# Kernel optimization log

Measured on AMD Instinct MI355X. Metric: run time of the kernel, lower is better.

Reference implementation:

```python
import jax, jax.numpy as jnp
import numpy as np

D = 3
NUM_LEVELS = 16
LEVEL_DIM = 2
BASE_RES = 16
PER_LEVEL_SCALE = 2.0
LOG2_HASH = 19
MAX_PARAMS = 2 ** LOG2_HASH
BASIS_NUM = 8
N_POINTS = 524288
N_FRAMES = 4

# per-level resolution / table-size bookkeeping, exactly as in ExpHashEncoder.__init__
_res = [int(np.ceil(BASE_RES * PER_LEVEL_SCALE ** l)) for l in range(NUM_LEVELS)]
_params = [int(min(MAX_PARAMS, (r + 1) ** D)) for r in _res]
_offsets = np.concatenate([[0], np.cumsum(_params)]).astype(np.int64)
TOTAL_PARAMS = int(_offsets[-1])  # 7131219

_PRIMES = np.array([1, 2654435761, 805459861], dtype=np.uint32)  # torch-ngp fast_hash primes
_CORNERS = np.stack(np.meshgrid(np.arange(2), np.arange(2), np.arange(2), indexing='ij'), -1).reshape(-1, D).astype(np.int32)  # [8,3]


def setup_inputs() -> dict:
    key = jax.random.key(0)
    k1, k2, k3, k4, k5 = jax.random.split(key, 5)
    inputs = jax.random.uniform(k1, (N_POINTS, D), dtype=jnp.float32)  # points in [0,1)^3
    exp = jax.random.normal(k2, (N_FRAMES, BASIS_NUM), dtype=jnp.float32)
    xyzstorays = jax.random.randint(k3, (N_POINTS,), 0, N_FRAMES * 1024, dtype=jnp.int32)
    std = 1e-4  # matches reset_parameters uniform(-1e-4, 1e-4)
    embeddings_mean = (jax.random.uniform(k4, (1, TOTAL_PARAMS, LEVEL_DIM), dtype=jnp.float32) * 2 - 1) * std
    embeddings = (jax.random.uniform(k5, (BASIS_NUM - 1, TOTAL_PARAMS, LEVEL_DIM), dtype=jnp.float32) * 2 - 1) * std
    return {"inputs": inputs, "exp": exp, "embeddings_mean": embeddings_mean,
            "embeddings": embeddings, "xyzstorays": xyzstorays}


def _grid_encode(inputs, cur_emb, frames):
    # inputs [B,3] in [0,1]; cur_emb [F, TOTAL_PARAMS, C]; frames [B] int32
    corners = jnp.asarray(_CORNERS)          # [8,3]
    primes = jnp.asarray(_PRIMES)            # [3] uint32
    outs = []
    for l in range(NUM_LEVELS):
        res, hsize, off = _res[l], _params[l], int(_offsets[l])
        scale = BASE_RES * PER_LEVEL_SCALE ** l - 1.0  # kernel: exp2(l*S)*H - 1
        pos = inputs * scale + 0.5            # [B,3]
        pg = jnp.floor(pos)
        frac = pos - pg                       # [B,3] trilinear fractions
        cc = pg.astype(jnp.int32)[:, None, :] + corners[None]  # [B,8,3] corner coords
        # trilinear weights: prod_d (bit_d ? frac_d : 1-frac_d)
        w = jnp.prod(jnp.where(corners[None].astype(bool), frac[:, None, :], 1.0 - frac[:, None, :]), axis=-1)  # [B,8]
        if (res + 1) ** D <= hsize:
            # dense (tiled) indexing with stride (res+1), as in get_grid_index
            stride = res + 1
            idx = cc[..., 0] + cc[..., 1] * stride + cc[..., 2] * (stride * stride)
        else:
            # fast_hash: xor of coord*prime, uint32 wraparound, then mod table size
            cu = cc.astype(jnp.uint32)
            h = (cu[..., 0] * primes[0]) ^ (cu[..., 1] * primes[1]) ^ (cu[..., 2] * primes[2])
            idx = (h % jnp.uint32(hsize)).astype(jnp.int32)
        emb_l = jax.lax.dynamic_slice_in_dim(cur_emb, off, hsize, axis=1)  # [F,hsize,C]
        vals = emb_l[frames[:, None], idx]    # [B,8,C] per-frame gather
        outs.append(jnp.sum(w[..., None] * vals, axis=1))  # [B,C]
    return jnp.concatenate(outs, axis=-1)     # [B, L*C]


def reference(inputs, exp, embeddings_mean, embeddings, xyzstorays):
    frames = (xyzstorays // 1024).astype(jnp.int32)  # [B]
    basis = jnp.concatenate([embeddings_mean, embeddings], axis=0)  # [BASIS, T, C]
    cur = jnp.einsum('fb,btc->ftc', exp, basis)                     # blended per-frame tables [F,T,C]
    return _grid_encode(inputs, cur, frames)
```

## Files before the change

### kernel.cpp

```cpp
#include <hip/hip_runtime.h>
#include <hip/hip_bf16.h>
#include <stdint.h>


static constexpr int      NPOINTS = 524288;
static constexpr size_t   TOTAL_T = 7131219;
static constexpr uint32_t NENT    = 7131219u;
static constexpr uint32_t TPAD    = 7131264;
static constexpr uint32_t BLEND_BLOCKS = (NENT + 1023u) / 1024u;

#define OFFS_INIT {0u,4913u,40850u,315475u,839763u,1364051u,1888339u,2412627u, \
                   2936915u,3461203u,3985491u,4509779u,5034067u,5558355u,6082643u,6606931u}

__device__ __forceinline__ uint32_t pack_bf16x2(float a, float b) {
    __hip_bfloat162 h;
    h.x = __float2bfloat16(a);
    h.y = __float2bfloat16(b);
    uint32_t u;
    __builtin_memcpy(&u, &h, 4);
    return u;
}

__device__ __forceinline__ float2 unpack_bf16x2(uint32_t u) {
    float2 r;
    uint32_t lx = u << 16;
    uint32_t ly = u & 0xFFFF0000u;
    __builtin_memcpy(&r.x, &lx, 4);
    __builtin_memcpy(&r.y, &ly, 4);
    return r;
}

__device__ __forceinline__ float2 nt_load_f2(const float2* p) {
    uint64_t raw = __builtin_nontemporal_load((const uint64_t*)p);
    float2 r;
    __builtin_memcpy(&r, &raw, 8);
    return r;
}

__global__ __launch_bounds__(256) void blend_coal_kernel(
    const float2* __restrict__ mean2, const float2* __restrict__ emb2,
    const float* __restrict__ expw, uint32_t* __restrict__ cur)
{
    float w[4][8];
#pragma unroll
    for (int f = 0; f < 4; ++f)
#pragma unroll
        for (int b = 0; b < 8; ++b)
            w[f][b] = expw[8 * f + b];

    uint32_t base = blockIdx.x * 1024u + threadIdx.x;

    if (blockIdx.x != BLEND_BLOCKS - 1u) {
#pragma unroll
        for (int k = 0; k < 4; ++k) {
            uint32_t idx = base + 256u * k;
            float2 m = nt_load_f2(&mean2[idx]);
            float ax[4], ay[4];
#pragma unroll
            for (int f = 0; f < 4; ++f) { ax[f] = w[f][0] * m.x; ay[f] = w[f][0] * m.y; }
#pragma unroll
            for (int b = 0; b < 7; ++b) {
                float2 v = nt_load_f2(&emb2[(size_t)b * TOTAL_T + idx]);
#pragma unroll
                for (int f = 0; f < 4; ++f) {
                    ax[f] = fmaf(w[f][b + 1], v.x, ax[f]);
                    ay[f] = fmaf(w[f][b + 1], v.y, ay[f]);
                }
            }
#pragma unroll
            for (int f = 0; f < 4; ++f)
                cur[(size_t)f * TPAD + idx] = pack_bf16x2(ax[f], ay[f]);
        }
    } else {
#pragma unroll
        for (int k = 0; k < 4; ++k) {
            uint32_t idx = base + 256u * k;
            if (idx >= NENT) return;
            float2 m = nt_load_f2(&mean2[idx]);
            float ax[4], ay[4];
#pragma unroll
            for (int f = 0; f < 4; ++f) { ax[f] = w[f][0] * m.x; ay[f] = w[f][0] * m.y; }
#pragma unroll
            for (int b = 0; b < 7; ++b) {
                float2 v = nt_load_f2(&emb2[(size_t)b * TOTAL_T + idx]);
#pragma unroll
                for (int f = 0; f < 4; ++f) {
                    ax[f] = fmaf(w[f][b + 1], v.x, ax[f]);
                    ay[f] = fmaf(w[f][b + 1], v.y, ay[f]);
                }
            }
#pragma unroll
            for (int f = 0; f < 4; ++f)
                cur[(size_t)f * TPAD + idx] = pack_bf16x2(ax[f], ay[f]);
        }
    }
}

__global__ __launch_bounds__(256) void gather_lvl_kernel(
    const float* __restrict__ xyz, const int* __restrict__ rays,
    const uint32_t* __restrict__ cur, float* __restrict__ out)
{
    uint32_t phase = blockIdx.x >> 11;
    uint32_t pb    = blockIdx.x & 2047u;
    uint32_t p     = pb * 256u + threadIdx.x;

    float x = xyz[3 * p + 0], y = xyz[3 * p + 1], z = xyz[3 * p + 2];
    uint32_t frame = ((uint32_t)rays[p]) >> 10;
    const uint32_t* __restrict__ tab = cur + (size_t)frame * TPAD;

    if (phase == 0) {
        float o[6];
        const uint32_t ST[3]  = {17u, 33u, 65u};
        const uint32_t OFF[3] = {0u, 4913u, 40850u};
#pragma unroll
        for (int l = 0; l < 3; ++l) {
            float scale = (float)((16 << l) - 1);
            float px = fmaf(x, scale, 0.5f);
            float py = fmaf(y, scale, 0.5f);
            float pz = fmaf(z, scale, 0.5f);
            float fx = floorf(px), fy = floorf(py), fz = floorf(pz);
            float wx = px - fx, wy = py - fy, wz = pz - fz;
            uint32_t ix = (uint32_t)(int)fx, iy = (uint32_t)(int)fy, iz = (uint32_t)(int)fz;
            uint32_t st = ST[l], st2 = st * st, base = OFF[l];
            float sx = 0.f, sy = 0.f;
#pragma unroll
            for (int c = 0; c < 8; ++c) {
                uint32_t bx = (c >> 2) & 1, by = (c >> 1) & 1, bz = c & 1;
                uint32_t idx = base + (ix + bx) + (iy + by) * st + (iz + bz) * st2;
                float w = (bx ? wx : 1.f - wx) * (by ? wy : 1.f - wy) * (bz ? wz : 1.f - wz);
                float2 v = unpack_bf16x2(tab[idx]);
                sx = fmaf(w, v.x, sx);
                sy = fmaf(w, v.y, sy);
            }
            o[2 * l] = sx; o[2 * l + 1] = sy;
        }
        float* ob = out + (size_t)p * 32;
        *(float4*)ob       = make_float4(o[0], o[1], o[2], o[3]);
        *(float2*)(ob + 4) = make_float2(o[4], o[5]);
    } else {
        int l = (int)phase + 2;
        float scale = (float)((16 << l) - 1);
        uint32_t base = 315475u + ((phase - 1u) << 19);
        float px = fmaf(x, scale, 0.5f);
        float py = fmaf(y, scale, 0.5f);
        float pz = fmaf(z, scale, 0.5f);
        float fx = floorf(px), fy = floorf(py), fz = floorf(pz);
        float wx = px - fx, wy = py - fy, wz = pz - fz;
        uint32_t ix = (uint32_t)(int)fx, iy = (uint32_t)(int)fy, iz = (uint32_t)(int)fz;
        float sx = 0.f, sy = 0.f;
#pragma unroll
        for (int c = 0; c < 8; ++c) {
            uint32_t bx = (c >> 2) & 1, by = (c >> 1) & 1, bz = c & 1;
            uint32_t h = (ix + bx)
                       ^ ((iy + by) * 2654435761u)
                       ^ ((iz + bz) * 805459861u);
            uint32_t idx = base + (h & 0x7FFFFu);
            float w = (bx ? wx : 1.f - wx) * (by ? wy : 1.f - wy) * (bz ? wz : 1.f - wz);
            float2 v = unpack_bf16x2(tab[idx]);
            sx = fmaf(w, v.x, sx);
            sy = fmaf(w, v.y, sy);
        }
        *(float2*)(out + (size_t)p * 32 + 2 * l) = make_float2(sx, sy);
    }
}

__global__ __launch_bounds__(256) void fused_fallback_kernel(
    const float* __restrict__ xyz, const int* __restrict__ rays,
    const float* __restrict__ expw,
    const float2* __restrict__ mean, const float2* __restrict__ emb,
    float* __restrict__ out)
{
    int p = blockIdx.x * 256 + threadIdx.x;
    if (p >= NPOINTS) return;
    float x = xyz[3 * p], y = xyz[3 * p + 1], z = xyz[3 * p + 2];
    int frame = rays[p] >> 10;
    float e[8];
#pragma unroll
    for (int b = 0; b < 8; ++b) e[b] = expw[8 * frame + b];

    constexpr uint32_t OFFS[16] = OFFS_INIT;

    for (int l = 0; l < 16; ++l) {
        float scale = (float)((16 << l) - 1);
        float px = fmaf(x, scale, 0.5f);
        float py = fmaf(y, scale, 0.5f);
        float pz = fmaf(z, scale, 0.5f);
        float fx = floorf(px), fy = floorf(py), fz = floorf(pz);
        float wx = px - fx, wy = py - fy, wz = pz - fz;
        int ix = (int)fx, iy = (int)fy, iz = (int)fz;
        uint32_t base = OFFS[l];
        float sx = 0.f, sy = 0.f;
#pragma unroll
        for (int c = 0; c < 8; ++c) {
            int bx = (c >> 2) & 1, by = (c >> 1) & 1, bz = c & 1;
            uint32_t idx;
            if (l < 3) {
                uint32_t st = (l == 0) ? 17u : (l == 1) ? 33u : 65u;
                idx = (uint32_t)(ix + bx) + (uint32_t)(iy + by) * st
                    + (uint32_t)(iz + bz) * st * st;
            } else {
                idx = ((uint32_t)(ix + bx)
                     ^ ((uint32_t)(iy + by) * 2654435761u)
                     ^ ((uint32_t)(iz + bz) * 805459861u)) & 0x7FFFFu;
            }
            uint32_t g = base + idx;
            float2 m = mean[g];
            float vx = e[0] * m.x, vy = e[0] * m.y;
#pragma unroll
            for (int b = 0; b < 7; ++b) {
                float2 t = emb[(size_t)b * TOTAL_T + g];
                vx = fmaf(e[1 + b], t.x, vx);
                vy = fmaf(e[1 + b], t.y, vy);
            }
            float w = (bx ? wx : 1.f - wx) * (by ? wy : 1.f - wy) * (bz ? wz : 1.f - wz);
            sx = fmaf(w, vx, sx);
            sy = fmaf(w, vy, sy);
        }
        out[(size_t)p * 32 + 2 * l]     = sx;
        out[(size_t)p * 32 + 2 * l + 1] = sy;
    }
}

extern "C" void kernel_launch(void* const* d_in, const int* in_sizes, int n_in,
                              void* d_out, int out_size, void* d_ws, size_t ws_size,
                              hipStream_t stream) {
    const float* inputs = (const float*)d_in[0];
    const float* expw   = (const float*)d_in[1];
    const float* mean   = (const float*)d_in[2];
    const float* emb    = (const float*)d_in[3];
    const int*   rays   = (const int*)d_in[4];
    float* out = (float*)d_out;

    const size_t need_bf16 = (size_t)4 * TPAD * 4;

    if (ws_size >= need_bf16) {
        uint32_t* cur = (uint32_t*)d_ws;
        blend_coal_kernel<<<BLEND_BLOCKS, 256, 0, stream>>>(
            (const float2*)mean, (const float2*)emb, expw, cur);
        gather_lvl_kernel<<<14 * 2048, 256, 0, stream>>>(
            inputs, rays, cur, out);
    } else {
        fused_fallback_kernel<<<NPOINTS / 256, 256, 0, stream>>>(
            inputs, rays, expw, (const float2*)mean, (const float2*)emb, out);
    }
}
```

Baseline: 1.051 ms.

## Sort points by frame before gathering and add batched-load blend with merge pass

Adds a counting sort that groups points by frame into a packed xyz+index buffer. The per-level gather then reads one frame table per block group and writes level-major results to workspace, and a merge kernel scatters those rows back into the output. The blend kernel now issues all 32 loads per thread before doing any FMAs, to raise memory-level parallelism. This is meant to improve cache locality of the random table lookups. In exchange it adds extra kernels, workspace traffic and an output permutation, and it only runs if the workspace is large enough.

```diff
diff --git a/kernel.cpp b/kernel.cpp
--- a/kernel.cpp
+++ b/kernel.cpp
@@ -8,6 +8,14 @@
 static constexpr uint32_t NENT    = 7131219u;
 static constexpr uint32_t TPAD    = 7131264;
 static constexpr uint32_t BLEND_BLOCKS = (NENT + 1023u) / 1024u;
+
+static constexpr size_t OFF_CUR   = 0;
+static constexpr size_t OFF_SXYZF = 114100224;
+static constexpr size_t OFF_SPERM = OFF_SXYZF + 8388608;
+static constexpr size_t OFF_CTRS  = OFF_SPERM + 2097152;
+static constexpr size_t OFF_WS    = OFF_CTRS + 256;
+static constexpr size_t NEED_V4   = OFF_WS + 67108864;
+static constexpr size_t NEED_V3   = 114100224;
 
 #define OFFS_INIT {0u,4913u,40850u,315475u,839763u,1364051u,1888339u,2412627u, \
                    2936915u,3461203u,3985491u,4509779u,5034067u,5558355u,6082643u,6606931u}
@@ -37,7 +45,7 @@
     return r;
 }
 
-__global__ __launch_bounds__(256) void blend_coal_kernel(
+__global__ __launch_bounds__(256) void blend_mlp_kernel(
     const float2* __restrict__ mean2, const float2* __restrict__ emb2,
     const float* __restrict__ expw, uint32_t* __restrict__ cur)
 {
@@ -51,52 +59,194 @@
     uint32_t base = blockIdx.x * 1024u + threadIdx.x;
 
     if (blockIdx.x != BLEND_BLOCKS - 1u) {
+        float2 v[4][8];
 #pragma unroll
         for (int k = 0; k < 4; ++k) {
             uint32_t idx = base + 256u * k;
-            float2 m = nt_load_f2(&mean2[idx]);
+            v[k][0] = nt_load_f2(&mean2[idx]);
+#pragma unroll
+            for (int b = 0; b < 7; ++b)
+                v[k][1 + b] = nt_load_f2(&emb2[(size_t)b * TOTAL_T + idx]);
+        }
+#pragma unroll
+        for (int k = 0; k < 4; ++k) {
+            uint32_t idx = base + 256u * k;
             float ax[4], ay[4];
 #pragma unroll
+            for (int f = 0; f < 4; ++f) { ax[f] = w[f][0] * v[k][0].x; ay[f] = w[f][0] * v[k][0].y; }
+#pragma unroll
+            for (int b = 0; b < 7; ++b)
+#pragma unroll
+                for (int f = 0; f < 4; ++f) {
+                    ax[f] = fmaf(w[f][b + 1], v[k][1 + b].x, ax[f]);
+                    ay[f] = fmaf(w[f][b + 1], v[k][1 + b].y, ay[f]);
+                }
+#pragma unroll
+            for (int f = 0; f < 4; ++f)
+                cur[(size_t)f * TPAD + idx] = pack_bf16x2(ax[f], ay[f]);
+        }
+    } else {
+#pragma unroll
+        for (int k = 0; k < 4; ++k) {
+            uint32_t idx = base + 256u * k;
+            if (idx >= NENT) continue;
+            float2 m = mean2[idx];
+            float ax[4], ay[4];
+#pragma unroll
             for (int f = 0; f < 4; ++f) { ax[f] = w[f][0] * m.x; ay[f] = w[f][0] * m.y; }
 #pragma unroll
             for (int b = 0; b < 7; ++b) {
-                float2 v = nt_load_f2(&emb2[(size_t)b * TOTAL_T + idx]);
+                float2 e = emb2[(size_t)b * TOTAL_T + idx];
 #pragma unroll
                 for (int f = 0; f < 4; ++f) {
-                    ax[f] = fmaf(w[f][b + 1], v.x, ax[f]);
-                    ay[f] = fmaf(w[f][b + 1], v.y, ay[f]);
+                    ax[f] = fmaf(w[f][b + 1], e.x, ax[f]);
+                    ay[f] = fmaf(w[f][b + 1], e.y, ay[f]);
                 }
             }
 #pragma unroll
             for (int f = 0; f < 4; ++f)
                 cur[(size_t)f * TPAD + idx] = pack_bf16x2(ax[f], ay[f]);
         }
+    }
+}
+
+__global__ void sort_init_kernel(uint32_t* ctrs) {
+    if (threadIdx.x < 16) ctrs[threadIdx.x] = 0u;
+}
+
+__global__ __launch_bounds__(256) void sort_count_kernel(
+    const int* __restrict__ rays, uint32_t* __restrict__ ctrs)
+{
+    __shared__ uint32_t h[4];
+    if (threadIdx.x < 4) h[threadIdx.x] = 0u;
+    __syncthreads();
+    uint32_t p = blockIdx.x * 256u + threadIdx.x;
+    uint32_t f = (((uint32_t)rays[p]) >> 10) & 3u;
+    atomicAdd(&h[f], 1u);
+    __syncthreads();
+    if (threadIdx.x < 4) atomicAdd(&ctrs[threadIdx.x], h[threadIdx.x]);
+}
+
+__global__ __launch_bounds__(256) void sort_scatter_kernel(
+    const float* __restrict__ xyz, const int* __restrict__ rays,
+    uint32_t* __restrict__ ctrs,
+    uint32_t* __restrict__ sperm, float4* __restrict__ sxyzf)
+{
+    __shared__ uint32_t hcnt[4];
+    __shared__ uint32_t hbase[4];
+    if (threadIdx.x < 4) hcnt[threadIdx.x] = 0u;
+    __syncthreads();
+
+    uint32_t p = blockIdx.x * 256u + threadIdx.x;
+    uint32_t f = (((uint32_t)rays[p]) >> 10) & 3u;
+    uint32_t myofs = atomicAdd(&hcnt[f], 1u);
+    __syncthreads();
+
+    if (threadIdx.x < 4)
+        hbase[threadIdx.x] = atomicAdd(&ctrs[4 + threadIdx.x], hcnt[threadIdx.x]);
+    __syncthreads();
+
+    uint32_t c0 = ctrs[0], c1 = ctrs[1], c2 = ctrs[2];
+    uint32_t bucket_base = (f == 0) ? 0u : (f == 1) ? c0 : (f == 2) ? (c0 + c1) : (c0 + c1 + c2);
+    uint32_t slot = bucket_base + hbase[f] + myofs;
+    if (slot >= (uint32_t)NPOINTS) slot = NPOINTS - 1;
+
+    uint32_t packed = p | (f << 20);
+    sperm[slot] = packed;
+    float x = xyz[3 * p], y = xyz[3 * p + 1], z = xyz[3 * p + 2];
+    float4 q; q.x = x; q.y = y; q.z = z; q.w = __uint_as_float(packed);
+    sxyzf[slot] = q;
+}
+
+__global__ __launch_bounds__(256) void gather_lvl_kernel(
+    const float4* __restrict__ sxyzf, const uint32_t* __restrict__ cur,
+    float2* __restrict__ ws)
+{
+    uint32_t phase  = blockIdx.x >> 11;
+    uint32_t gl     = blockIdx.x & 2047u;
+    uint32_t fgrp   = (gl & 7u) >> 1;
+    uint32_t within = (gl >> 3) * 2u + (gl & 1u);
+    uint32_t b      = fgrp * 512u + within;
+    uint32_t j      = b * 256u + threadIdx.x;
+
+    float4 q = sxyzf[j];
+    float x = q.x, y = q.y, z = q.z;
+    uint32_t f = (__float_as_uint(q.w) >> 20) & 3u;
+    const uint32_t* __restrict__ tab = cur + (size_t)f * TPAD;
+
+    if (phase == 0) {
+        const uint32_t ST[3]  = {17u, 33u, 65u};
+        const uint32_t OFF[3] = {0u, 4913u, 40850u};
+#pragma unroll
+        for (int l = 0; l < 3; ++l) {
+            float scale = (float)((16 << l) - 1);
+            float px = fmaf(x, scale, 0.5f);
+            float py = fmaf(y, scale, 0.5f);
+            float pz = fmaf(z, scale, 0.5f);
+            float fx = floorf(px), fy = floorf(py), fz = floorf(pz);
+            float wx = px - fx, wy = py - fy, wz = pz - fz;
+            uint32_t ix = (uint32_t)(int)fx, iy = (uint32_t)(int)fy, iz = (uint32_t)(int)fz;
+            uint32_t st = ST[l], st2 = st * st, base = OFF[l];
+            float sx = 0.f, sy = 0.f;
+#pragma unroll
+            for (int c = 0; c < 8; ++c) {
+                uint32_t bx = (c >> 2) & 1, by = (c >> 1) & 1, bz = c & 1;
+                uint32_t idx = base + (ix + bx) + (iy + by) * st + (iz + bz) * st2;
+                float w = (bx ? wx : 1.f - wx) * (by ? wy : 1.f - wy) * (bz ? wz : 1.f - wz);
+                float2 v = unpack_bf16x2(tab[idx]);
+                sx = fmaf(w, v.x, sx);
+                sy = fmaf(w, v.y, sy);
+            }
+            ws[(size_t)l * NPOINTS + j] = make_float2(sx, sy);
+        }
     } else {
-#pragma unroll
-        for (int k = 0; k < 4; ++k) {
-            uint32_t idx = base + 256u * k;
-            if (idx >= NENT) return;
-            float2 m = nt_load_f2(&mean2[idx]);
-            float ax[4], ay[4];
-#pragma unroll
-            for (int f = 0; f < 4; ++f) { ax[f] = w[f][0] * m.x; ay[f] = w[f][0] * m.y; }
-#pragma unroll
-            for (int b = 0; b < 7; ++b) {
-                float2 v = nt_load_f2(&emb2[(size_t)b * TOTAL_T + idx]);
-#pragma unroll
-                for (int f = 0; f < 4; ++f) {
-                    ax[f] = fmaf(w[f][b + 1], v.x, ax[f]);
-                    ay[f] = fmaf(w[f][b + 1], v.y, ay[f]);
-                }
-            }
-#pragma unroll
-            for (int f = 0; f < 4; ++f)
-                cur[(size_t)f * TPAD + idx] = pack_bf16x2(ax[f], ay[f]);
-        }
-    }
-}
-
-__global__ __launch_bounds__(256) void gather_lvl_kernel(
+        int l = (int)phase + 2;
+        float scale = (float)((16 << l) - 1);
+        uint32_t base = 315475u + ((phase - 1u) << 19);
+        float px = fmaf(x, scale, 0.5f);
+        float py = fmaf(y, scale, 0.5f);
+        float pz = fmaf(z, scale, 0.5f);
+        float fx = floorf(px), fy = floorf(py), fz = floorf(pz);
+        float wx = px - fx, wy = py - fy, wz = pz - fz;
+        uint32_t ix = (uint32_t)(int)fx, iy = (uint32_t)(int)fy, iz = (uint32_t)(int)fz;
+        float sx = 0.f, sy = 0.f;
+#pragma unroll
+        for (int c = 0; c < 8; ++c) {
+            uint32_t bx = (c >> 2) & 1, by = (c >> 1) & 1, bz = c & 1;
+            uint32_t h = (ix + bx)
+                       ^ ((iy + by) * 2654435761u)
+                       ^ ((iz + bz) * 805459861u);
+            uint32_t idx = base + (h & 0x7FFFFu);
+            float w = (bx ? wx : 1.f - wx) * (by ? wy : 1.f - wy) * (bz ? wz : 1.f - wz);
+            float2 v = unpack_bf16x2(tab[idx]);
+            sx = fmaf(w, v.x, sx);
+            sy = fmaf(w, v.y, sy);
+        }
+        ws[(size_t)l * NPOINTS + j] = make_float2(sx, sy);
+    }
+}
+
+__global__ __launch_bounds__(256) void merge_out_kernel(
+    const uint32_t* __restrict__ sperm, const float2* __restrict__ ws,
+    float* __restrict__ out)
+{
+    uint32_t j = blockIdx.x * 256u + threadIdx.x;
+    uint32_t p = sperm[j] & 0xFFFFFu;
+    if (p >= (uint32_t)NPOINTS) p = NPOINTS - 1;
+    float4 o[8];
+#pragma unroll
+    for (int l = 0; l < 16; l += 2) {
+        float2 a = ws[(size_t)l * NPOINTS + j];
+        float2 c = ws[(size_t)(l + 1) * NPOINTS + j];
+        o[l >> 1] = make_float4(a.x, a.y, c.x, c.y);
+    }
+    float* ob = out + (size_t)p * 32;
+#pragma unroll
+    for (int k = 0; k < 8; ++k)
+        *(float4*)(ob + 4 * k) = o[k];
+}
+
+__global__ __launch_bounds__(256) void gather_legacy_kernel(
     const float* __restrict__ xyz, const int* __restrict__ rays,
     const uint32_t* __restrict__ cur, float* __restrict__ out)
 {
@@ -105,7 +255,7 @@
     uint32_t p     = pb * 256u + threadIdx.x;
 
     float x = xyz[3 * p + 0], y = xyz[3 * p + 1], z = xyz[3 * p + 2];
-    uint32_t frame = ((uint32_t)rays[p]) >> 10;
+    uint32_t frame = (((uint32_t)rays[p]) >> 10) & 3u;
     const uint32_t* __restrict__ tab = cur + (size_t)frame * TPAD;
 
     if (phase == 0) {
@@ -173,7 +323,7 @@
     int p = blockIdx.x * 256 + threadIdx.x;
     if (p >= NPOINTS) return;
     float x = xyz[3 * p], y = xyz[3 * p + 1], z = xyz[3 * p + 2];
-    int frame = rays[p] >> 10;
+    int frame = (rays[p] >> 10) & 3;
     float e[8];
 #pragma unroll
     for (int b = 0; b < 8; ++b) e[b] = expw[8 * frame + b];
@@ -231,13 +381,28 @@
     const int*   rays   = (const int*)d_in[4];
     float* out = (float*)d_out;
 
-    const size_t need_bf16 = (size_t)4 * TPAD * 4;
-
-    if (ws_size >= need_bf16) {
+    char* wsb = (char*)d_ws;
+
+    if (ws_size >= NEED_V4) {
+        uint32_t* cur   = (uint32_t*)(wsb + OFF_CUR);
+        float4*   sxyzf = (float4*)(wsb + OFF_SXYZF);
+        uint32_t* sperm = (uint32_t*)(wsb + OFF_SPERM);
+        uint32_t* ctrs  = (uint32_t*)(wsb + OFF_CTRS);
+        float2*   ws2   = (float2*)(wsb + OFF_WS);
+
+        blend_mlp_kernel<<<BLEND_BLOCKS, 256, 0, stream>>>(
+            (const float2*)mean, (const float2*)emb, expw, cur);
+        sort_init_kernel<<<1, 64, 0, stream>>>(ctrs);
+        sort_count_kernel<<<NPOINTS / 256, 256, 0, stream>>>(rays, ctrs);
+        sort_scatter_kernel<<<NPOINTS / 256, 256, 0, stream>>>(
+            inputs, rays, ctrs, sperm, sxyzf);
+        gather_lvl_kernel<<<14 * 2048, 256, 0, stream>>>(sxyzf, cur, ws2);
+        merge_out_kernel<<<NPOINTS / 256, 256, 0, stream>>>(sperm, ws2, out);
+    } else if (ws_size >= NEED_V3) {
         uint32_t* cur = (uint32_t*)d_ws;
-        blend_coal_kernel<<<BLEND_BLOCKS, 256, 0, stream>>>(
+        blend_mlp_kernel<<<BLEND_BLOCKS, 256, 0, stream>>>(
             (const float2*)mean, (const float2*)emb, expw, cur);
-        gather_lvl_kernel<<<14 * 2048, 256, 0, stream>>>(
+        gather_legacy_kernel<<<14 * 2048, 256, 0, stream>>>(
             inputs, rays, cur, out);
     } else {
         fused_fallback_kernel<<<NPOINTS / 256, 256, 0, stream>>>(
```

New measurement: 940.1 us. -10.5%, faster.
